# Performance work log

Hardware: AMD Instinct MI355X
Metric: run time of the kernel (lower is better)

Reference implementation:

```python
import jax, jax.numpy as jnp
import numpy as np

B, S, D, H = 16, 577, 768, 12  # batch, seq (24*24+1 cls), hidden, heads
WH, WW = 24, 24
HEAD = D // H
NUM_REL = (2 * WH - 1) * (2 * WW - 1) + 3  # 2212


def make_rel_pos_index(wh, ww):
    # mirrors TFData2VecVisionRelativePositionBias.get_position_index
    xx, yy = np.meshgrid(np.arange(wh), np.arange(ww))  # 'xy' indexing like tf.meshgrid
    coords = np.stack([yy, xx], axis=0).reshape(2, -1)  # [2, wh*ww]
    rel = coords[:, :, None] - coords[:, None, :]       # [2, N, N]
    rel = rel.transpose(1, 2, 0)                        # [N, N, 2]
    rx = (rel[:, :, 0] + wh - 1) * (2 * ww - 1)
    ry = rel[:, :, 1] + ww - 1
    idx = rx + ry                                       # [N, N]
    n = idx.shape[0]
    top = np.full((1, n), NUM_REL - 3, dtype=idx.dtype)
    left = np.full((n, 1), NUM_REL - 2, dtype=idx.dtype)
    corner = np.full((1, 1), NUM_REL - 1, dtype=idx.dtype)
    idx = np.concatenate([top, idx], axis=0)
    idx = np.concatenate([np.concatenate([corner, left], axis=0), idx], axis=1)
    return idx.astype(np.int32)  # [N+1, N+1]


def setup_inputs() -> dict:
    key = jax.random.key(0)
    ks = jax.random.split(key, 6)
    scale = 0.02
    return {
        "hidden_states": jax.random.normal(ks[0], (B, S, D), jnp.float32),
        "Wq": jax.random.normal(ks[1], (D, D), jnp.float32) * scale,
        "bq": jnp.zeros((D,), jnp.float32),
        "Wk": jax.random.normal(ks[2], (D, D), jnp.float32) * scale,
        "Wv": jax.random.normal(ks[3], (D, D), jnp.float32) * scale,
        "bv": jnp.zeros((D,), jnp.float32),
        "rel_pos_bias_table": jax.random.normal(ks[4], (NUM_REL, H), jnp.float32) * scale,
        "rel_pos_index": jnp.asarray(make_rel_pos_index(WH, WW)),
    }


def reference(hidden_states, Wq, bq, Wk, Wv, bv, rel_pos_bias_table, rel_pos_index):
    b, s, _ = hidden_states.shape
    q = (hidden_states @ Wq + bq).reshape(b, s, H, HEAD).transpose(0, 2, 1, 3)
    k = (hidden_states @ Wk).reshape(b, s, H, HEAD).transpose(0, 2, 1, 3)
    v = (hidden_states @ Wv + bv).reshape(b, s, H, HEAD).transpose(0, 2, 1, 3)
    scores = jnp.einsum("bhqd,bhkd->bhqk", q, k) / jnp.sqrt(jnp.float32(HEAD))
    # gathered relative position bias: [S, S, H] -> [H, S, S]
    bias = rel_pos_bias_table[rel_pos_index].transpose(2, 0, 1)
    scores = scores + bias[None]
    probs = jax.nn.softmax(scores, axis=-1)
    out = jnp.einsum("bhqk,bhkd->bhqd", probs, v)
    out = out.transpose(0, 2, 1, 3).reshape(b, s, D)
    return out
```

## Files before the change

### kernel.cpp

```cpp
#include <hip/hip_runtime.h>
#include <hip/hip_bf16.h>


typedef __attribute__((ext_vector_type(8))) short bf16x8;
typedef __attribute__((ext_vector_type(4))) float f32x4;
typedef unsigned short u16;

#define SEQ 577
#define MTOT 9232
#define QKV_STRIDE 7090176
#define VT_PITCH 640
#define BT_K 584
#define BT_Q 632

static __device__ __forceinline__ u16 f2bf(float x) {
  unsigned int u = __float_as_uint(x);
  u = (u + 0x7FFFu + ((u >> 16) & 1u)) >> 16;
  return (u16)u;
}
static __device__ __forceinline__ float bf2f(u16 v) {
  return __uint_as_float(((unsigned int)v) << 16);
}

static __device__ __forceinline__ void gload_lds16(const void* g, void* l) {
  __builtin_amdgcn_global_load_lds(
      (const __attribute__((address_space(1))) unsigned int*)g,
      (__attribute__((address_space(3))) unsigned int*)l, 16, 0, 0);
}

__global__ __launch_bounds__(256) void prep(
    const float* __restrict__ Wq, const float* __restrict__ Wk,
    const float* __restrict__ Wv, const float* __restrict__ X,
    u16* __restrict__ WT, u16* __restrict__ Xb) {
  const int bid = blockIdx.x;
  if (bid < 1728) {
    __shared__ float t[32][33];
    const int z = bid / 576;
    const int rem = bid - z * 576;
    const int kx = rem % 24, ny = rem / 24;
    const float* W = (z == 0) ? Wq : (z == 1) ? Wk : Wv;
    int x = threadIdx.x & 31;
    int y = threadIdx.x >> 5;
    int k0 = kx * 32;
    int n0 = ny * 32;
#pragma unroll
    for (int i = 0; i < 4; ++i)
      t[y + i * 8][x] = W[(size_t)(k0 + y + i * 8) * 768 + n0 + x];
    __syncthreads();
    u16* o = WT + (size_t)z * 589824;
#pragma unroll
    for (int i = 0; i < 4; ++i)
      o[(size_t)(n0 + y + i * 8) * 768 + k0 + x] = f2bf(t[x][y + i * 8]);
  } else {
    size_t i = ((size_t)(bid - 1728) * 256 + threadIdx.x) * 8;
    if (i >= (size_t)MTOT * 768) return;
    const float4* xp = (const float4*)(X + i);
    float4 a = xp[0], b = xp[1];
    u16 pk[8] = {f2bf(a.x), f2bf(a.y), f2bf(a.z), f2bf(a.w),
                 f2bf(b.x), f2bf(b.y), f2bf(b.z), f2bf(b.w)};
    *(int4*)(Xb + i) = *(const int4*)pk;
  }
}

__global__ __launch_bounds__(256) void prep2(
    const u16* __restrict__ v,
    u16* __restrict__ vT,
    const float* __restrict__ table, const int* __restrict__ idx,
    u16* __restrict__ biasT) {
  const int bid = blockIdx.x;
  const int tid = threadIdx.x;
  if (bid < 960) {
    const int tile = bid % 5;
    const int bh = bid / 5;
    const int b = bh / 12, h = bh % 12;
    __shared__ u16 T[128][64];
    const int s0 = tile * 128;
    const u16* vp = v + (size_t)b * SEQ * 768 + h * 64;
#pragma unroll
    for (int it = 0; it < 4; ++it) {
      int c = tid + it * 256;
      int r = c >> 3, ko = (c & 7) << 3;
      int gs = s0 + r;
      int4 val = make_int4(0, 0, 0, 0);
      if (gs < SEQ) val = *(const int4*)(vp + (size_t)gs * 768 + ko);
      *(int4*)&T[r][ko ^ (((r >> 3) & 7) << 3)] = val;
    }
    __syncthreads();
    u16* op = vT + (size_t)bh * 64 * VT_PITCH;
#pragma unroll
    for (int it = 0; it < 4; ++it) {
      int c = tid + it * 256;
      int d = c >> 4, so = (c & 15) << 3;
      u16 tmp[8];
#pragma unroll
      for (int j = 0; j < 8; ++j) {
        int rr = so + j;
        tmp[j] = T[rr][d ^ (((rr >> 3) & 7) << 3)];
      }
      *(int4*)(op + (size_t)d * VT_PITCH + s0 + so) = *(const int4*)tmp;
    }
  } else {
    const int r = bid - 960;
    const int k = r % BT_K;
    const int h = r / BT_K;
    u16* op = biasT + ((size_t)h * BT_K + k) * BT_Q;
    for (int q = tid; q < BT_Q; q += 256) {
      u16 vv = 0;
      if (q < SEQ && k < SEQ) vv = f2bf(table[idx[q * SEQ + k] * 12 + h]);
      op[q] = vv;
    }
  }
}

#define G_STAGE_A(BS, KT, U)                                                   \
  gload_lds16(aptr[(U)] + (KT) * 32, &SAB[(BS)][((U) * 128 + w16) * 32])
#define G_STAGE_B(BS, KT, U)                                                   \
  gload_lds16(bptr + (size_t)(U) * 128 * 768 + (KT) * 32,                      \
              &SAB[(BS)][8192 + ((U) * 128 + w16) * 32])

__global__ __launch_bounds__(512, 2) void qkv_gemm(
    const u16* __restrict__ Xb,
    const u16* __restrict__ WT,
    const float* __restrict__ bq, const float* __restrict__ bv,
    u16* __restrict__ qkv) {
  const int bid = blockIdx.x;
  const int x = bid & 7;
  const int l = bid >> 3;
  const int mt = x + 8 * (l / 6);
  if (mt >= 37) return;
  const int nt = l % 6;
  const int m0 = mt * 256;
  const int widx = nt >> 1;
  const int nb = (nt & 1) * 384;

  const int tid = threadIdx.x;
  const int lane = tid & 63;
  const int w = tid >> 6;
  const int wm2 = w >> 2;
  const int wn = w & 3;
  const int quad = lane >> 4;
  const int l15 = lane & 15;
  const int w16 = w * 16;

  __shared__ u16 SAB[3][20480];

  const int srow = w16 + (lane >> 2);
  const int ce8 = (((lane & 3) ^ ((lane >> 3) & 3))) * 8;
  const u16* aptr[2];
#pragma unroll
  for (int u = 0; u < 2; ++u) {
    int rr = m0 + u * 128 + srow;
    if (rr > MTOT - 1) rr = MTOT - 1;
    aptr[u] = Xb + (size_t)rr * 768 + ce8;
  }
  const u16* bptr =
      WT + (size_t)widx * 589824 + (size_t)(nb + srow) * 768 + ce8;

  const int ca8 = (quad ^ ((l15 >> 1) & 3)) * 8;

  f32x4 acc[8][6];
#pragma unroll
  for (int i = 0; i < 8; ++i)
#pragma unroll
    for (int j = 0; j < 6; ++j) acc[i][j] = (f32x4){0.f, 0.f, 0.f, 0.f};
  bf16x8 af[4], bfr[6];

  G_STAGE_A(0, 0, 0); G_STAGE_A(0, 0, 1);
  G_STAGE_B(0, 0, 0); G_STAGE_B(0, 0, 1); G_STAGE_B(0, 0, 2);
  G_STAGE_A(1, 1, 0); G_STAGE_A(1, 1, 1);
  G_STAGE_B(1, 1, 0); G_STAGE_B(1, 1, 1); G_STAGE_B(1, 1, 2);
  asm volatile("s_waitcnt vmcnt(5)" ::: "memory");
  __builtin_amdgcn_s_barrier();
  asm volatile("" ::: "memory");

  int bs = 0, bt2 = 2;
  for (int t = 0; t < 24; ++t) {
#pragma unroll
    for (int i = 0; i < 4; ++i)
      af[i] = *(const bf16x8*)&SAB[bs][(wm2 * 128 + i * 16 + l15) * 32 + ca8];
#pragma unroll
    for (int j = 0; j < 6; ++j)
      bfr[j] = *(const bf16x8*)&SAB[bs][8192 + (wn * 96 + j * 16 + l15) * 32 + ca8];
    if (t <= 21) { G_STAGE_A(bt2, t + 2, 0); G_STAGE_A(bt2, t + 2, 1); G_STAGE_B(bt2, t + 2, 0); }
    asm volatile("" ::: "memory");
    __builtin_amdgcn_s_barrier();
    asm volatile("s_waitcnt lgkmcnt(0)" ::: "memory");
    __builtin_amdgcn_s_setprio(1);
#pragma unroll
    for (int j = 0; j < 6; ++j)
#pragma unroll
      for (int i = 0; i < 4; ++i)
        acc[i][j] = __builtin_amdgcn_mfma_f32_16x16x32_bf16(af[i], bfr[j],
                                                            acc[i][j], 0, 0, 0);
    __builtin_amdgcn_s_setprio(0);
    asm volatile("" ::: "memory");
    __builtin_amdgcn_s_barrier();
    asm volatile("" ::: "memory");
#pragma unroll
    for (int i = 0; i < 4; ++i)
      af[i] = *(const bf16x8*)&SAB[bs][(wm2 * 128 + 64 + i * 16 + l15) * 32 + ca8];
#pragma unroll
    for (int j = 0; j < 6; ++j)
      bfr[j] = *(const bf16x8*)&SAB[bs][8192 + (wn * 96 + j * 16 + l15) * 32 + ca8];
    if (t <= 21) { G_STAGE_B(bt2, t + 2, 1); G_STAGE_B(bt2, t + 2, 2); }
    asm volatile("" ::: "memory");
    __builtin_amdgcn_s_barrier();
    asm volatile("s_waitcnt lgkmcnt(0)" ::: "memory");
    __builtin_amdgcn_s_setprio(1);
#pragma unroll
    for (int j = 0; j < 6; ++j)
#pragma unroll
      for (int i = 0; i < 4; ++i)
        acc[4 + i][j] = __builtin_amdgcn_mfma_f32_16x16x32_bf16(
            af[i], bfr[j], acc[4 + i][j], 0, 0, 0);
    __builtin_amdgcn_s_setprio(0);
    if (t < 22) {
      asm volatile("s_waitcnt vmcnt(5)" ::: "memory");
    } else if (t == 22) {
      asm volatile("s_waitcnt vmcnt(0)" ::: "memory");
    }
    asm volatile("" ::: "memory");
    __builtin_amdgcn_s_barrier();
    asm volatile("" ::: "memory");
    bs = (bs == 2) ? 0 : bs + 1;
    bt2 = (bt2 == 2) ? 0 : bt2 + 1;
  }

  const float scale = (widx == 0) ? 0.125f : 1.0f;
  float biasv[6];
#pragma unroll
  for (int nf = 0; nf < 6; ++nf) {
    int n = nb + wn * 96 + nf * 16 + l15;
    biasv[nf] = (widx == 0) ? bq[n] * 0.125f : (widx == 2) ? bv[n] : 0.f;
  }
  u16* E = &SAB[0][0];
  u16* ob = qkv + (size_t)widx * QKV_STRIDE + nb;
#pragma unroll
  for (int half = 0; half < 2; ++half) {
    if (wm2 == half) {
#pragma unroll
      for (int mf = 0; mf < 8; ++mf)
#pragma unroll
        for (int nf = 0; nf < 6; ++nf)
#pragma unroll
          for (int r = 0; r < 4; ++r) {
            int rowl = mf * 16 + quad * 4 + r;
            int col = wn * 96 + nf * 16 + l15;
            int colr = (((col >> 4) ^ quad) << 4) | (col & 15);
            E[rowl * 384 + colr] = f2bf(acc[mf][nf][r] * scale + biasv[nf]);
          }
    }
    __syncthreads();
#pragma unroll 4
    for (int it = 0; it < 12; ++it) {
      int c = it * 512 + tid;
      int row = c / 48;
      int ch = c - row * 48;
      int m = m0 + half * 128 + row;
      if (m < MTOT) {
        int g = (ch >> 1) ^ ((row >> 2) & 3);
        int colr = (g << 4) + (ch & 1) * 8;
        *(int4*)(ob + (size_t)m * 768 + ch * 8) = *(const int4*)&E[row * 384 + colr];
      }
    }
    __syncthreads();
  }
}

__global__ __launch_bounds__(512) void attn(
    const u16* __restrict__ qk, const u16* __restrict__ vT,
    const u16* __restrict__ biasT, float* __restrict__ out) {
  const int bh = blockIdx.x;
  const int qt = blockIdx.y;
  const int b = bh / 12, h = bh - b * 12;
  const int tid = threadIdx.x;
  const int lane = tid & 63;
  const int w = tid >> 6;
  const int quad = lane >> 4;
  const int l15 = lane & 15;

  const u16* qp = qk + (size_t)b * SEQ * 768 + h * 64;
  const u16* kp = qp + (size_t)QKV_STRIDE;
  const u16* vtp = vT + (size_t)bh * 64 * VT_PITCH;
  const u16* btp = biasT + (size_t)h * BT_K * BT_Q;

  __shared__ u16 Ks[64][72];
  __shared__ u16 VTs[64][72];
  __shared__ u16 Ps[8][16][72];

  const int qrow0 = qt * 128 + w * 16;

  bf16x8 qf[2];
  {
    int row = qrow0 + l15;
    if (row > 576) row = 576;
    qf[0] = *(const bf16x8*)(qp + (size_t)row * 768 + quad * 8);
    qf[1] = *(const bf16x8*)(qp + (size_t)row * 768 + 32 + quad * 8);
  }
  int qb = qrow0 + quad * 4;
  if (qb > 576) qb = 576;

  const int rr = tid >> 3, ko = (tid & 7) << 3;

  float lacc[4] = {0.f, 0.f, 0.f, 0.f};
  f32x4 O[4];
#pragma unroll
  for (int dt = 0; dt < 4; ++dt) O[dt] = (f32x4){0.f, 0.f, 0.f, 0.f};

  int4 pk_k, pk_v;
  short4 pb[4];
  {
    int gk = rr;
    pk_k = make_int4(0, 0, 0, 0);
    if (gk < SEQ) pk_k = *(const int4*)(kp + (size_t)gk * 768 + ko);
    pk_v = *(const int4*)(vtp + (size_t)rr * VT_PITCH + ko);
#pragma unroll
    for (int nt = 0; nt < 4; ++nt) {
      int kb = nt * 16 + l15;
      if (kb > 576) kb = 576;
      pb[nt] = *(const short4*)(btp + (size_t)kb * BT_Q + qb);
    }
  }

  for (int kt = 0; kt < 10; ++kt) {
    const int kbase = kt * 64;
    *(int4*)&Ks[rr][ko] = pk_k;
    *(int4*)&VTs[rr][ko] = pk_v;
    __syncthreads();

    f32x4 zz[4];
#pragma unroll
    for (int nt = 0; nt < 4; ++nt)
      zz[nt] = (f32x4){bf2f((u16)pb[nt].x), bf2f((u16)pb[nt].y),
                       bf2f((u16)pb[nt].z), bf2f((u16)pb[nt].w)};

    if (kt < 9) {
      const int nk = kbase + 64;
      int gk = nk + rr;
      pk_k = make_int4(0, 0, 0, 0);
      if (gk < SEQ) pk_k = *(const int4*)(kp + (size_t)gk * 768 + ko);
      pk_v = *(const int4*)(vtp + (size_t)rr * VT_PITCH + nk + ko);
#pragma unroll
      for (int nt = 0; nt < 4; ++nt) {
        int kb = nk + nt * 16 + l15;
        if (kb > 576) kb = 576;
        pb[nt] = *(const short4*)(btp + (size_t)kb * BT_Q + qb);
      }
    }

    f32x4 s[4];
#pragma unroll
    for (int nt = 0; nt < 4; ++nt) {
      f32x4 z = zz[nt];
      bf16x8 kf0 = *(const bf16x8*)(&Ks[nt * 16 + l15][quad * 8]);
      bf16x8 kf1 = *(const bf16x8*)(&Ks[nt * 16 + l15][32 + quad * 8]);
      z = __builtin_amdgcn_mfma_f32_16x16x32_bf16(qf[0], kf0, z, 0, 0, 0);
      z = __builtin_amdgcn_mfma_f32_16x16x32_bf16(qf[1], kf1, z, 0, 0, 0);
      s[nt] = z;
    }

    const bool full = (kbase + 64 <= SEQ);
#pragma unroll
    for (int nt = 0; nt < 4; ++nt) {
#pragma unroll
      for (int r = 0; r < 4; ++r) {
        float p = __expf(s[nt][r]);
        unsigned int u = __float_as_uint(p);
        float pt = __uint_as_float(u & 0xFFFF0000u);
        if (full) lacc[r] += pt;
        else lacc[r] += ((kbase + nt * 16 + l15) < SEQ) ? pt : 0.f;
        Ps[w][quad * 4 + r][((nt ^ quad) << 4) + l15] = (u16)(u >> 16);
      }
    }

#pragma unroll
    for (int ks = 0; ks < 2; ++ks) {
      int cc = (ks * 32 + quad * 8) ^ ((l15 >> 2) << 4);
      bf16x8 pf = *(const bf16x8*)(&Ps[w][l15][cc]);
#pragma unroll
      for (int dt = 0; dt < 4; ++dt) {
        bf16x8 vf = *(const bf16x8*)(&VTs[dt * 16 + l15][ks * 32 + quad * 8]);
        O[dt] = __builtin_amdgcn_mfma_f32_16x16x32_bf16(pf, vf, O[dt], 0, 0, 0);
      }
    }
    __syncthreads();
  }

#pragma unroll
  for (int r = 0; r < 4; ++r) {
    float l = lacc[r];
    l += __shfl_xor(l, 1);
    l += __shfl_xor(l, 2);
    l += __shfl_xor(l, 4);
    l += __shfl_xor(l, 8);
    int row = qrow0 + quad * 4 + r;
    if (row < SEQ) {
      float inv = 1.f / l;
#pragma unroll
      for (int dt = 0; dt < 4; ++dt)
        out[((size_t)(b * SEQ + row)) * 768 + h * 64 + dt * 16 + l15] = O[dt][r] * inv;
    }
  }
}

extern "C" void kernel_launch(void* const* d_in, const int* in_sizes, int n_in,
                              void* d_out, int out_size, void* d_ws, size_t ws_size,
                              hipStream_t stream) {
  const float* hs = (const float*)d_in[0];
  const float* Wq = (const float*)d_in[1];
  const float* bq = (const float*)d_in[2];
  const float* Wk = (const float*)d_in[3];
  const float* Wv = (const float*)d_in[4];
  const float* bv = (const float*)d_in[5];
  const float* table = (const float*)d_in[6];
  const int* idx = (const int*)d_in[7];
  float* out = (float*)d_out;

  char* ws = (char*)d_ws;
  u16* qkv = (u16*)ws;
  u16* WT = (u16*)(ws + 42541056);
  u16* Xb = (u16*)(ws + 46080000);
  u16* vT = (u16*)(ws + 42541056);
  u16* biasT = (u16*)(ws + 58269696);

  hipLaunchKernelGGL(prep, dim3(5190), dim3(256), 0, stream, Wq, Wk, Wv, hs, WT, Xb);
  hipLaunchKernelGGL(qkv_gemm, dim3(240), dim3(512), 0, stream, Xb, WT, bq, bv, qkv);
  hipLaunchKernelGGL(prep2, dim3(7968), dim3(256), 0, stream,
                     qkv + 2 * (size_t)QKV_STRIDE, vT, table, idx, biasT);
  hipLaunchKernelGGL(attn, dim3(192, 5), dim3(512), 0, stream, qkv, vT, biasT, out);
}
```

Baseline: 223.6 us.

## Store relative-position bias query-major and drop register prefetch in attention

```diff
diff --git a/kernel.cpp b/kernel.cpp
--- a/kernel.cpp
+++ b/kernel.cpp
@@ -10,8 +10,7 @@
 #define MTOT 9232
 #define QKV_STRIDE 7090176
 #define VT_PITCH 640
-#define BT_K 584
-#define BT_Q 632
+#define B_PITCH 640
 
 static __device__ __forceinline__ u16 f2bf(float x) {
   unsigned int u = __float_as_uint(x);
@@ -66,7 +65,7 @@
     const u16* __restrict__ v,
     u16* __restrict__ vT,
     const float* __restrict__ table, const int* __restrict__ idx,
-    u16* __restrict__ biasT) {
+    u16* __restrict__ biasm) {
   const int bid = blockIdx.x;
   const int tid = threadIdx.x;
   if (bid < 960) {
@@ -101,13 +100,12 @@
     }
   } else {
     const int r = bid - 960;
-    const int k = r % BT_K;
-    const int h = r / BT_K;
-    u16* op = biasT + ((size_t)h * BT_K + k) * BT_Q;
-    for (int q = tid; q < BT_Q; q += 256) {
+    const int q = r % 577;
+    const int h = r / 577;
+    for (int k = tid; k < B_PITCH; k += 256) {
       u16 vv = 0;
-      if (q < SEQ && k < SEQ) vv = f2bf(table[idx[q * SEQ + k] * 12 + h]);
-      op[q] = vv;
+      if (k < SEQ) vv = f2bf(table[idx[q * SEQ + k] * 12 + h]);
+      biasm[((size_t)h * SEQ + q) * B_PITCH + k] = vv;
     }
   }
 }
@@ -269,7 +267,7 @@
 
 __global__ __launch_bounds__(512) void attn(
     const u16* __restrict__ qk, const u16* __restrict__ vT,
-    const u16* __restrict__ biasT, float* __restrict__ out) {
+    const u16* __restrict__ biasm, float* __restrict__ out) {
   const int bh = blockIdx.x;
   const int qt = blockIdx.y;
   const int b = bh / 12, h = bh - b * 12;
@@ -282,7 +280,7 @@
   const u16* qp = qk + (size_t)b * SEQ * 768 + h * 64;
   const u16* kp = qp + (size_t)QKV_STRIDE;
   const u16* vtp = vT + (size_t)bh * 64 * VT_PITCH;
-  const u16* btp = biasT + (size_t)h * BT_K * BT_Q;
+  const u16* bp = biasm + (size_t)h * SEQ * B_PITCH;
 
   __shared__ u16 Ks[64][72];
   __shared__ u16 VTs[64][72];
@@ -297,61 +295,43 @@
     qf[0] = *(const bf16x8*)(qp + (size_t)row * 768 + quad * 8);
     qf[1] = *(const bf16x8*)(qp + (size_t)row * 768 + 32 + quad * 8);
   }
-  int qb = qrow0 + quad * 4;
-  if (qb > 576) qb = 576;
-
-  const int rr = tid >> 3, ko = (tid & 7) << 3;
+  int brow[4];
+#pragma unroll
+  for (int r = 0; r < 4; ++r) {
+    int rr = qrow0 + quad * 4 + r;
+    if (rr > 576) rr = 576;
+    brow[r] = rr;
+  }
 
   float lacc[4] = {0.f, 0.f, 0.f, 0.f};
   f32x4 O[4];
 #pragma unroll
   for (int dt = 0; dt < 4; ++dt) O[dt] = (f32x4){0.f, 0.f, 0.f, 0.f};
 
-  int4 pk_k, pk_v;
-  short4 pb[4];
-  {
-    int gk = rr;
-    pk_k = make_int4(0, 0, 0, 0);
-    if (gk < SEQ) pk_k = *(const int4*)(kp + (size_t)gk * 768 + ko);
-    pk_v = *(const int4*)(vtp + (size_t)rr * VT_PITCH + ko);
-#pragma unroll
-    for (int nt = 0; nt < 4; ++nt) {
-      int kb = nt * 16 + l15;
-      if (kb > 576) kb = 576;
-      pb[nt] = *(const short4*)(btp + (size_t)kb * BT_Q + qb);
-    }
-  }
-
   for (int kt = 0; kt < 10; ++kt) {
     const int kbase = kt * 64;
-    *(int4*)&Ks[rr][ko] = pk_k;
-    *(int4*)&VTs[rr][ko] = pk_v;
-    __syncthreads();
-
-    f32x4 zz[4];
+    u16 bb[4][4];
 #pragma unroll
     for (int nt = 0; nt < 4; ++nt)
-      zz[nt] = (f32x4){bf2f((u16)pb[nt].x), bf2f((u16)pb[nt].y),
-                       bf2f((u16)pb[nt].z), bf2f((u16)pb[nt].w)};
-
-    if (kt < 9) {
-      const int nk = kbase + 64;
-      int gk = nk + rr;
-      pk_k = make_int4(0, 0, 0, 0);
-      if (gk < SEQ) pk_k = *(const int4*)(kp + (size_t)gk * 768 + ko);
-      pk_v = *(const int4*)(vtp + (size_t)rr * VT_PITCH + nk + ko);
-#pragma unroll
-      for (int nt = 0; nt < 4; ++nt) {
-        int kb = nk + nt * 16 + l15;
-        if (kb > 576) kb = 576;
-        pb[nt] = *(const short4*)(btp + (size_t)kb * BT_Q + qb);
-      }
-    }
+#pragma unroll
+      for (int r = 0; r < 4; ++r)
+        bb[nt][r] = bp[(size_t)brow[r] * B_PITCH + kbase + nt * 16 + l15];
+
+    {
+      int rr = tid >> 3, ko = (tid & 7) << 3;
+      int gk = kbase + rr;
+      int4 kvv = make_int4(0, 0, 0, 0);
+      if (gk < SEQ) kvv = *(const int4*)(kp + (size_t)gk * 768 + ko);
+      *(int4*)&Ks[rr][ko] = kvv;
+      *(int4*)&VTs[rr][ko] = *(const int4*)(vtp + (size_t)rr * VT_PITCH + kbase + ko);
+    }
+    __syncthreads();
 
     f32x4 s[4];
 #pragma unroll
     for (int nt = 0; nt < 4; ++nt) {
-      f32x4 z = zz[nt];
+      f32x4 z = (f32x4){bf2f(bb[nt][0]), bf2f(bb[nt][1]),
+                        bf2f(bb[nt][2]), bf2f(bb[nt][3])};
       bf16x8 kf0 = *(const bf16x8*)(&Ks[nt * 16 + l15][quad * 8]);
       bf16x8 kf1 = *(const bf16x8*)(&Ks[nt * 16 + l15][32 + quad * 8]);
       z = __builtin_amdgcn_mfma_f32_16x16x32_bf16(qf[0], kf0, z, 0, 0, 0);
@@ -421,11 +401,11 @@
   u16* WT = (u16*)(ws + 42541056);
   u16* Xb = (u16*)(ws + 46080000);
   u16* vT = (u16*)(ws + 42541056);
-  u16* biasT = (u16*)(ws + 58269696);
+  u16* biasm = (u16*)(ws + 58269696);
 
   hipLaunchKernelGGL(prep, dim3(5190), dim3(256), 0, stream, Wq, Wk, Wv, hs, WT, Xb);
   hipLaunchKernelGGL(qkv_gemm, dim3(240), dim3(512), 0, stream, Xb, WT, bq, bv, qkv);
-  hipLaunchKernelGGL(prep2, dim3(7968), dim3(256), 0, stream,
-                     qkv + 2 * (size_t)QKV_STRIDE, vT, table, idx, biasT);
-  hipLaunchKernelGGL(attn, dim3(192, 5), dim3(512), 0, stream, qkv, vT, biasT, out);
-}
+  hipLaunchKernelGGL(prep2, dim3(7884), dim3(256), 0, stream,
+                     qkv + 2 * (size_t)QKV_STRIDE, vT, table, idx, biasm);
+  hipLaunchKernelGGL(attn, dim3(192, 5), dim3(512), 0, stream, qkv, vT, biasm, out);
+}
```

Result: faster. 195.4 us (-12.6%).
